# Kernel optimization log

Hardware: AMD Instinct MI355X
Metric: run time of the kernel (lower is better)

Reference implementation:

```python
import jax, jax.numpy as jnp
import numpy as np
import math

D_MODEL = 1024
D_STATE = 128
D_CONV = 4
EXPAND = 2
HEADDIM = 64
NGROUPS = 1
CHUNK = 256
D_INNER = EXPAND * D_MODEL
D_SSM = D_INNER
NHEADS = D_SSM // HEADDIM
CONV_DIM = D_SSM + 2 * NGROUPS * D_STATE
D_IN_PROJ = 2 * D_INNER + 2 * NGROUPS * D_STATE + NHEADS
BATCH = 2
SEQLEN = 4096
EPS = 1e-5


def segsum(x):
    # x: (..., T) -> (..., T, T); segsum[i, j] = sum_{j < k <= i} x[k], -inf above diagonal
    T = x.shape[-1]
    xc = jnp.cumsum(x, axis=-1)
    d = xc[..., :, None] - xc[..., None, :]
    mask = jnp.tril(jnp.ones((T, T), dtype=bool))
    return jnp.where(mask, d, -jnp.inf)


def setup_inputs() -> dict:
    key = jax.random.key(0)
    ks = jax.random.split(key, 8)
    u = jax.random.normal(ks[0], (BATCH, SEQLEN, D_MODEL), jnp.float32)
    W_in = jax.random.normal(ks[1], (D_IN_PROJ, D_MODEL), jnp.float32) / np.sqrt(D_MODEL)
    conv_w = jax.random.uniform(ks[2], (CONV_DIM, D_CONV), jnp.float32, -1.0, 1.0) / np.sqrt(D_CONV)
    conv_b = jnp.zeros((CONV_DIM,), jnp.float32)
    # dt_bias init as in the torch module: inverse-softplus of dt ~ LogUniform(1e-3, 1e-1)
    dt = jnp.exp(jax.random.uniform(ks[3], (NHEADS,), jnp.float32) * (math.log(0.1) - math.log(0.001)) + math.log(0.001))
    dt = jnp.maximum(dt, 1e-4)
    dt_bias = dt + jnp.log(-jnp.expm1(-dt))
    A_log = jnp.log(jax.random.uniform(ks[4], (NHEADS,), jnp.float32, 1.0, 16.0))
    D = jnp.ones((NHEADS,), jnp.float32)
    norm_w = jnp.ones((D_SSM,), jnp.float32)
    W_out = jax.random.normal(ks[5], (D_MODEL, D_INNER), jnp.float32) / np.sqrt(D_INNER)
    return {"u": u, "W_in": W_in, "conv_w": conv_w, "conv_b": conv_b,
            "dt_bias": dt_bias, "A_log": A_log, "D": D, "norm_w": norm_w, "W_out": W_out}


def reference(u, W_in, conv_w, conv_b, dt_bias, A_log, D, norm_w, W_out):
    b, L, _ = u.shape
    zxbcdt = u @ W_in.T  # (b, L, d_in_proj); d_mlp == 0 for this config
    z, xBC, dt = jnp.split(zxbcdt, [D_SSM, D_SSM + CONV_DIM], axis=-1)

    # depthwise causal conv1d + SiLU (kernel width D_CONV, left padding)
    xpad = jnp.pad(xBC, ((0, 0), (D_CONV - 1, 0), (0, 0)))
    acc = conv_b
    for k in range(D_CONV):
        acc = acc + xpad[:, k:k + L, :] * conv_w[:, k]
    xBC = jax.nn.silu(acc)

    x, Bm, Cm = jnp.split(xBC, [D_SSM, D_SSM + NGROUPS * D_STATE], axis=-1)
    hpg = NHEADS // NGROUPS  # heads per B/C group
    Bh = jnp.repeat(Bm.reshape(b, L, NGROUPS, D_STATE), hpg, axis=2)  # (b, L, h, n)
    Ch = jnp.repeat(Cm.reshape(b, L, NGROUPS, D_STATE), hpg, axis=2)
    x = x.reshape(b, L, NHEADS, HEADDIM)

    dt = jax.nn.softplus(dt + dt_bias)  # (b, L, h)
    A = -jnp.exp(A_log)  # (h,)

    # ---- SSD chunked selective scan ----
    nc = L // CHUNK
    xc = x.reshape(b, nc, CHUNK, NHEADS, HEADDIM)
    Bc = Bh.reshape(b, nc, CHUNK, NHEADS, D_STATE)
    Cc = Ch.reshape(b, nc, CHUNK, NHEADS, D_STATE)
    dt_bclh = dt.reshape(b, nc, CHUNK, NHEADS)
    dA = jnp.transpose(dt_bclh, (0, 3, 1, 2)) * A[None, :, None, None]  # (b, h, c, l)
    A_cs = jnp.cumsum(dA, axis=-1)  # (b, h, c, l)

    # intra-chunk (diagonal block) outputs
    Ldiag = jnp.exp(segsum(dA))  # (b, h, c, l, s)
    x_dt = xc * dt_bclh[..., None]  # fold dt into x
    Y_diag = jnp.einsum('bclhn,bcshn,bhcls,bcshp->bclhp', Cc, Bc, Ldiag, x_dt)

    # per-chunk final states
    decay_states = jnp.exp(A_cs[..., -1:] - A_cs)  # (b, h, c, l)
    states = jnp.einsum('bclhn,bhcl,bclhp->bchpn', Bc, decay_states, x_dt)

    # inter-chunk recurrence via segsum over chunk-level decays
    chunk_sum = jnp.pad(A_cs[..., -1], ((0, 0), (0, 0), (1, 0)))  # (b, h, c+1)
    decay_chunk = jnp.exp(segsum(chunk_sum))  # (b, h, c+1, c+1)
    states = jnp.concatenate([jnp.zeros_like(states[:, :1]), states], axis=1)
    new_states = jnp.einsum('bhzc,bchpn->bzhpn', decay_chunk, states)
    prev_states = new_states[:, :-1]  # state entering each chunk

    # state -> output contribution
    Y_off = jnp.einsum('bclhn,bchpn,bhcl->bclhp', Cc, prev_states, jnp.exp(A_cs))

    y = (Y_diag + Y_off).reshape(b, L, NHEADS, HEADDIM) + x * D[None, None, :, None]
    y = y.reshape(b, L, D_SSM)

    # gated RMSNorm (norm_before_gate=False, ngroups=1 -> full-dim norm)
    y = y * jax.nn.silu(z)
    y = y * jax.lax.rsqrt(jnp.mean(jnp.square(y), axis=-1, keepdims=True) + EPS) * norm_w
    return y @ W_out.T
```

## Files before the change

### kernel.cpp

```cpp
#include <hip/hip_runtime.h>
#include <hip/hip_bf16.h>

#define ZX_LD   4384
#define XC_LD   2304
#define NH      32
#define HD      64
#define DS      128
#define CHK     256
#define NC      16
#define LTOT    4096
#define ROWS    8192
#define DSSM    2048
#define YPAD    80

typedef __bf16 bf16_t;
typedef bf16_t bf16x8 __attribute__((ext_vector_type(8)));
typedef float  f32x4  __attribute__((ext_vector_type(4)));
typedef unsigned short u16x8 __attribute__((ext_vector_type(8)));
typedef unsigned short u16x4 __attribute__((ext_vector_type(4)));

__device__ inline float bf2f(unsigned short u) {
  unsigned int x = ((unsigned int)u) << 16;
  float f; __builtin_memcpy(&f, &x, 4); return f;
}

#define GLOAD_LDS16(gp, lp) \
  __builtin_amdgcn_global_load_lds((const __attribute__((address_space(1))) void*)(gp), \
                                   (__attribute__((address_space(3))) void*)(lp), 16, 0, 0)

__global__ __launch_bounds__(256) void cast_f32_bf16(
    const float* __restrict__ in, bf16_t* __restrict__ out,
    long nvalid, long total)
{
  const long e0 = ((long)blockIdx.x * 256 + threadIdx.x) * 8;
  if (e0 >= total) return;
  bf16x8 o;
  if (e0 + 8 <= nvalid) {
    const float4 a = *(const float4*)(in + e0);
    const float4 b = *(const float4*)(in + e0 + 4);
    o[0]=(bf16_t)a.x; o[1]=(bf16_t)a.y; o[2]=(bf16_t)a.z; o[3]=(bf16_t)a.w;
    o[4]=(bf16_t)b.x; o[5]=(bf16_t)b.y; o[6]=(bf16_t)b.z; o[7]=(bf16_t)b.w;
  } else {
#pragma unroll
    for (int j = 0; j < 8; ++j) o[j] = (bf16_t)0.f;
  }
  *(bf16x8*)(out + e0) = o;
}

__global__ __launch_bounds__(256) void gemm_bt_mfma(
    const bf16_t* __restrict__ A, const bf16_t* __restrict__ B,
    float* __restrict__ C, int M, int N, int K,
    int lda, int ldb, int ldc)
{
  __shared__ __align__(16) bf16_t As[128 * 32];
  __shared__ __align__(16) bf16_t Bs[128 * 32];
  const int tid  = threadIdx.x;
  const int lane = tid & 63;
  const int wave = tid >> 6;
  const int bm = blockIdx.y * 128;
  const int bn = blockIdx.x * 128;
  const int wr = (wave >> 1) * 64;
  const int wc = (wave & 1) * 64;

  const int c0   = wave * 2;
  const int lrow = lane >> 2;
  const int lcol = (lane & 3) * 8;
  const bf16_t* Ag0 = A + (size_t)(bm + c0 * 16 + lrow) * lda + lcol;
  const bf16_t* Ag1 = A + (size_t)(bm + c0 * 16 + 16 + lrow) * lda + lcol;
  const bf16_t* Bg0 = B + (size_t)(bn + c0 * 16 + lrow) * ldb + lcol;
  const bf16_t* Bg1 = B + (size_t)(bn + c0 * 16 + 16 + lrow) * ldb + lcol;
  bf16_t* Al0 = As + c0 * 512;
  bf16_t* Al1 = As + c0 * 512 + 512;
  bf16_t* Bl0 = Bs + c0 * 512;
  bf16_t* Bl1 = Bs + c0 * 512 + 512;

  f32x4 acc[4][4];
#pragma unroll
  for (int i = 0; i < 4; ++i)
#pragma unroll
    for (int j = 0; j < 4; ++j) acc[i][j] = (f32x4){0.f, 0.f, 0.f, 0.f};

  const int nk = K >> 5;
  for (int kt = 0; kt < nk; ++kt) {
    const int k0 = kt * 32;
    __syncthreads();
    GLOAD_LDS16(Ag0 + k0, Al0);
    GLOAD_LDS16(Ag1 + k0, Al1);
    GLOAD_LDS16(Bg0 + k0, Bl0);
    GLOAD_LDS16(Bg1 + k0, Bl1);
    __syncthreads();

    const bf16_t* Ab = As + (wr + (lane & 15)) * 32 + (lane >> 4) * 8;
    const bf16_t* Bb = Bs + (wc + (lane & 15)) * 32 + (lane >> 4) * 8;
    bf16x8 af[4], bfv[4];
#pragma unroll
    for (int mi = 0; mi < 4; ++mi) af[mi]  = *(const bf16x8*)(Ab + mi * 512);
#pragma unroll
    for (int ni = 0; ni < 4; ++ni) bfv[ni] = *(const bf16x8*)(Bb + ni * 512);
#pragma unroll
    for (int mi = 0; mi < 4; ++mi)
#pragma unroll
      for (int ni = 0; ni < 4; ++ni)
        acc[mi][ni] = __builtin_amdgcn_mfma_f32_16x16x32_bf16(af[mi], bfv[ni], acc[mi][ni], 0, 0, 0);
  }

  const int crow0 = bm + wr + (lane >> 4) * 4;
  const int ccol0 = bn + wc + (lane & 15);
#pragma unroll
  for (int ni = 0; ni < 4; ++ni) {
    const int ccol = ccol0 + ni * 16;
    if (ccol < N) {
#pragma unroll
      for (int mi = 0; mi < 4; ++mi) {
#pragma unroll
        for (int j = 0; j < 4; ++j) {
          C[(size_t)(crow0 + mi * 16 + j) * ldc + ccol] = acc[mi][ni][j];
        }
      }
    }
  }
}

__global__ __launch_bounds__(256) void conv_silu_kernel(
    const float* __restrict__ zx, const float* __restrict__ cw,
    const float* __restrict__ cb, bf16_t* __restrict__ xconv)
{
  const int ch  = blockIdx.x * 256 + threadIdx.x;
  const int row = blockIdx.y;
  const int l   = row & (LTOT - 1);
  float acc = cb[ch];
#pragma unroll
  for (int k = 0; k < 4; ++k) {
    const int ls = l - 3 + k;
    if (ls >= 0) acc = fmaf(zx[(size_t)(row - 3 + k) * ZX_LD + 2048 + ch], cw[ch*4 + k], acc);
  }
  const float r = acc / (1.f + __expf(-acc));
  xconv[(size_t)row * XC_LD + ch] = (bf16_t)r;
}

__global__ __launch_bounds__(256) void dt_kernel(
    const float* __restrict__ zx, const float* __restrict__ dtb,
    float* __restrict__ dtv)
{
  const int idx = blockIdx.x * 256 + threadIdx.x;
  const int row = idx >> 5;
  const int hh  = idx & 31;
  const float x = zx[(size_t)row * ZX_LD + 4352 + hh] + dtb[hh];
  dtv[idx] = (x > 20.f) ? x : log1pf(__expf(x));
}

__global__ __launch_bounds__(256) void chunk_states_kernel(
    const float* __restrict__ dtv, const float* __restrict__ A_log,
    const bf16_t* __restrict__ xconv,
    float* __restrict__ acs, float* __restrict__ totals,
    float* __restrict__ states)
{
  const int bid = blockIdx.x;
  const int h = bid & 31;
  const int c = (bid >> 5) & 15;
  const int b = bid >> 9;
  const int rowbase = b * LTOT + c * CHK;
  const int l = threadIdx.x;

  __shared__ float sWdt[256];
  __shared__ float wsum[4];
  __shared__ float xw[64][68];
  __shared__ float Bsh[64][132];

  const float dt = dtv[(size_t)(rowbase + l) * NH + h];
  const float Ah = -__expf(A_log[h]);
  float v = dt * Ah;
#pragma unroll
  for (int off = 1; off < 64; off <<= 1) {
    float up = __shfl_up(v, off, 64);
    if ((l & 63) >= off) v += up;
  }
  if ((l & 63) == 63) wsum[l >> 6] = v;
  __syncthreads();
  const float w0 = wsum[0], w1 = wsum[1], w2 = wsum[2], w3 = wsum[3];
  const int wid = l >> 6;
  float base = 0.f;
  if (wid > 0) base += w0;
  if (wid > 1) base += w1;
  if (wid > 2) base += w2;
  const float acsl  = v + base;
  const float total = w0 + w1 + w2 + w3;
  acs[bid * 256 + l] = acsl;
  if (l == 0) totals[(b * 32 + h) * 16 + c] = total;
  sWdt[l] = __expf(total - acsl) * dt;

  const int tx = l & 15;
  const int ty = l >> 4;
  const int r  = l >> 2;
  float acc[4][8];
#pragma unroll
  for (int i = 0; i < 4; ++i)
#pragma unroll
    for (int j = 0; j < 8; ++j) acc[i][j] = 0.f;

  for (int ls = 0; ls < 4; ++ls) {
    const int l0 = ls * 64;
    __syncthreads();
    {
      const float wgt = sWdt[l0 + r];
      const bf16_t* xrow = xconv + (size_t)(rowbase + l0 + r) * XC_LD + h * HD + (l & 3) * 16;
      float* xd = &xw[r][(l & 3) * 16];
      const u16x8* xp = (const u16x8*)xrow;
#pragma unroll
      for (int q = 0; q < 2; ++q) {
        u16x8 t = xp[q];
#pragma unroll
        for (int j = 0; j < 8; ++j) xd[q*8 + j] = bf2f(t[j]) * wgt;
      }
      const bf16_t* br = xconv + (size_t)(rowbase + l0 + r) * XC_LD + 2048 + (l & 3) * 32;
      float* bd = &Bsh[r][(l & 3) * 32];
      const u16x8* bp = (const u16x8*)br;
#pragma unroll
      for (int q = 0; q < 4; ++q) {
        u16x8 t = bp[q];
#pragma unroll
        for (int j = 0; j < 8; ++j) bd[q*8 + j] = bf2f(t[j]);
      }
    }
    __syncthreads();
#pragma unroll 8
    for (int s = 0; s < 64; ++s) {
      float4 pa = *(const float4*)&xw[s][ty*4];
      float4 b0 = *(const float4*)&Bsh[s][tx*4];
      float4 b1 = *(const float4*)&Bsh[s][64 + tx*4];
      float am[4] = {pa.x, pa.y, pa.z, pa.w};
      float bb[8] = {b0.x,b0.y,b0.z,b0.w,b1.x,b1.y,b1.z,b1.w};
#pragma unroll
      for (int i = 0; i < 4; ++i)
#pragma unroll
        for (int j = 0; j < 8; ++j) acc[i][j] = fmaf(am[i], bb[j], acc[i][j]);
    }
  }
  const size_t sbase = (size_t)bid * (HD * DS);
#pragma unroll
  for (int i = 0; i < 4; ++i) {
    const int p = ty * 4 + i;
#pragma unroll
    for (int j = 0; j < 8; ++j) {
      const int n = (j < 4) ? (tx*4 + j) : (64 + tx*4 + (j - 4));
      states[sbase + p * DS + n] = acc[i][j];
    }
  }
}

__global__ __launch_bounds__(256) void chunk_prefix_kernel(
    const float* __restrict__ st, const float* __restrict__ totals,
    bf16_t* __restrict__ prevbf)
{
  const int bh = blockIdx.x;
  const int b = bh >> 5;
  const int h = bh & 31;
  const int tid = threadIdx.x;
  float P[32];
#pragma unroll
  for (int e = 0; e < 32; ++e) P[e] = 0.f;
  for (int c = 0; c < NC; ++c) {
    const size_t base = (size_t)((b * 16 + c) * 32 + h) * (HD * DS);
    const float g = __expf(totals[bh * 16 + c]);
#pragma unroll
    for (int e = 0; e < 32; ++e) {
      const size_t idx = base + e * 256 + tid;
      prevbf[idx] = (bf16_t)P[e];
      P[e] = fmaf(P[e], g, st[idx]);
    }
  }
}

__global__ __launch_bounds__(256) void y_kernel_mfma(
    const bf16_t* __restrict__ xconv, const float* __restrict__ dtv,
    const float* __restrict__ acs,   const bf16_t* __restrict__ prevbf,
    const float* __restrict__ Dv,    float* __restrict__ ypre, int ypld)
{
  const int bid = blockIdx.x;
  const int lt = bid & 3;
  const int h  = (bid >> 2) & 31;
  const int c  = (bid >> 7) & 15;
  const int b  = bid >> 11;
  const int bch = (b * 16 + c) * 32 + h;
  const int rowbase = b * LTOT + c * CHK;
  const int tid  = threadIdx.x;
  const int lane = tid & 63;
  const int wv   = tid >> 6;
  const int ln15 = lane & 15;
  const int lg   = lane >> 4;

  __shared__ float sAcs[256];
  __shared__ float sDt[256];
  __shared__ __align__(16) bf16_t Cl[64 * 128];
  __shared__ __align__(16) bf16_t Bl[64 * 128];
  __shared__ __align__(16) bf16_t Sl[64 * YPAD];
  __shared__ __align__(16) bf16_t xT[64 * YPAD];
  unsigned short* xTu = (unsigned short*)xT;

  sAcs[tid] = acs[bch * 256 + tid];
  sDt[tid]  = dtv[(size_t)(rowbase + tid) * NH + h];

#pragma unroll
  for (int i = 0; i < 4; ++i) {
    const int chunk = wv * 4 + i;
    const int r  = chunk * 4 + lg;
    const int cs = ln15 ^ (r & 7);
    const bf16_t* src = xconv + (size_t)(rowbase + lt*64 + r) * XC_LD + 2176 + cs * 8;
    GLOAD_LDS16(src, Cl + chunk * 512);
  }
  __syncthreads();

  bf16x8 cf[4][4];
#pragma unroll
  for (int mi = 0; mi < 4; ++mi) {
    const int row = mi * 16 + ln15;
#pragma unroll
    for (int ks = 0; ks < 4; ++ks) {
      const int chunk = (ks * 4 + lg) ^ (row & 7);
      cf[mi][ks] = *(const bf16x8*)(Cl + row * 128 + chunk * 8);
    }
  }

  f32x4 acc[4];
#pragma unroll
  for (int mi = 0; mi < 4; ++mi) acc[mi] = (f32x4){0.f, 0.f, 0.f, 0.f};
  {
    const bf16_t* pb = prevbf + ((size_t)bch * 64 + 16 * wv + ln15) * 128 + lg * 8;
#pragma unroll
    for (int ks = 0; ks < 4; ++ks) {
      bf16x8 pf = *(const bf16x8*)(pb + ks * 32);
#pragma unroll
      for (int mi = 0; mi < 4; ++mi)
        acc[mi] = __builtin_amdgcn_mfma_f32_16x16x32_bf16(cf[mi][ks], pf, acc[mi], 0, 0, 0);
    }
  }
#pragma unroll
  for (int mi = 0; mi < 4; ++mi) {
#pragma unroll
    for (int j = 0; j < 4; ++j)
      acc[mi][j] *= __expf(sAcs[lt*64 + mi*16 + lg*4 + j]);
  }

  for (int st = 0; st <= lt; ++st) {
    __syncthreads();
#pragma unroll
    for (int i = 0; i < 4; ++i) {
      const int chunk = wv * 4 + i;
      const int r  = chunk * 4 + lg;
      const int cs = ln15 ^ (r & 7);
      const bf16_t* src = xconv + (size_t)(rowbase + st*64 + r) * XC_LD + 2048 + cs * 8;
      GLOAD_LDS16(src, Bl + chunk * 512);
    }
    {
      const int s  = tid >> 2;
      const int p0 = (tid & 3) * 16;
      const bf16_t* xr = xconv + (size_t)(rowbase + st*64 + s) * XC_LD + h * HD + p0;
      u16x8 v0 = *(const u16x8*)xr;
      u16x8 v1 = *(const u16x8*)(xr + 8);
#pragma unroll
      for (int j = 0; j < 8; ++j) xTu[(p0 + j) * YPAD + s] = v0[j];
#pragma unroll
      for (int j = 0; j < 8; ++j) xTu[(p0 + 8 + j) * YPAD + s] = v1[j];
    }
    __syncthreads();

    f32x4 sa[4];
#pragma unroll
    for (int mi = 0; mi < 4; ++mi) sa[mi] = (f32x4){0.f, 0.f, 0.f, 0.f};
    {
      const int row = 16 * wv + ln15;
#pragma unroll
      for (int ks = 0; ks < 4; ++ks) {
        const int chunk = (ks * 4 + lg) ^ (row & 7);
        bf16x8 bfr = *(const bf16x8*)(Bl + row * 128 + chunk * 8);
#pragma unroll
        for (int mi = 0; mi < 4; ++mi)
          sa[mi] = __builtin_amdgcn_mfma_f32_16x16x32_bf16(cf[mi][ks], bfr, sa[mi], 0, 0, 0);
      }
    }
    {
      const int sg = st * 64 + 16 * wv + ln15;
      const float as  = sAcs[sg];
      const float dts = sDt[sg];
#pragma unroll
      for (int mi = 0; mi < 4; ++mi) {
#pragma unroll
        for (int j = 0; j < 4; ++j) {
          const int lloc = mi * 16 + lg * 4 + j;
          const int ll = lt * 64 + lloc;
          float wvv = 0.f;
          if (ll >= sg) wvv = sa[mi][j] * __expf(sAcs[ll] - as) * dts;
          Sl[lloc * YPAD + 16 * wv + ln15] = (bf16_t)wvv;
        }
      }
    }
    __syncthreads();

#pragma unroll
    for (int ks2 = 0; ks2 < 2; ++ks2) {
      bf16x8 xf = *(const bf16x8*)(xT + (16 * wv + ln15) * YPAD + ks2 * 32 + lg * 8);
#pragma unroll
      for (int mi = 0; mi < 4; ++mi) {
        bf16x8 sf = *(const bf16x8*)(Sl + (mi * 16 + ln15) * YPAD + ks2 * 32 + lg * 8);
        acc[mi] = __builtin_amdgcn_mfma_f32_16x16x32_bf16(sf, xf, acc[mi], 0, 0, 0);
      }
    }
  }

  const float Dh = Dv[h];
  const int p = 16 * wv + ln15;
#pragma unroll
  for (int mi = 0; mi < 4; ++mi) {
#pragma unroll
    for (int j = 0; j < 4; ++j) {
      const int lloc = mi * 16 + lg * 4 + j;
      const int row  = rowbase + lt * 64 + lloc;
      const float xv = (float)xT[p * YPAD + lloc];
      ypre[(size_t)row * ypld + h * HD + p] = acc[mi][j] + xv * Dh;
    }
  }
}

__global__ __launch_bounds__(256) void rmsnorm_gate_kernel(
    const float* __restrict__ zx, const float* __restrict__ normw,
    bf16_t* __restrict__ ypre_bf)
{
  const int row = blockIdx.x;
  const int tid = threadIdx.x;
  float vals[8];
  float ss = 0.f;
#pragma unroll
  for (int e = 0; e < 8; ++e) {
    const int col = e * 256 + tid;
    const float y = zx[(size_t)row * ZX_LD + 2048 + col];
    const float z = zx[(size_t)row * ZX_LD + col];
    const float sz = z / (1.f + __expf(-z));
    const float v = y * sz;
    vals[e] = v;
    ss += v * v;
  }
#pragma unroll
  for (int off = 32; off >= 1; off >>= 1) ss += __shfl_xor(ss, off, 64);
  __shared__ float red[4];
  if ((tid & 63) == 0) red[tid >> 6] = ss;
  __syncthreads();
  const float tot = red[0] + red[1] + red[2] + red[3];
  const float scale = rsqrtf(tot / (float)DSSM + 1e-5f);
#pragma unroll
  for (int e = 0; e < 8; ++e) {
    const int col = e * 256 + tid;
    ypre_bf[(size_t)row * DSSM + col] = (bf16_t)(vals[e] * scale * normw[col]);
  }
}

extern "C" void kernel_launch(void* const* d_in, const int* in_sizes, int n_in,
                              void* d_out, int out_size, void* d_ws, size_t ws_size,
                              hipStream_t stream)
{
  const float* u       = (const float*)d_in[0];
  const float* W_in    = (const float*)d_in[1];
  const float* conv_w  = (const float*)d_in[2];
  const float* conv_b  = (const float*)d_in[3];
  const float* dt_bias = (const float*)d_in[4];
  const float* A_log   = (const float*)d_in[5];
  const float* Dv      = (const float*)d_in[6];
  const float* norm_w  = (const float*)d_in[7];
  const float* W_out   = (const float*)d_in[8];
  float* out = (float*)d_out;

  const size_t OFF_XC  = (size_t)ROWS * ZX_LD * 4;
  const size_t OFF_DT  = OFF_XC  + (size_t)ROWS * XC_LD * 2;
  const size_t OFF_ACS = OFF_DT  + (size_t)ROWS * NH * 4;
  const size_t OFF_TOT = OFF_ACS + (size_t)1024 * 256 * 4;
  const size_t OFF_ST  = OFF_TOT + 4096;
  const size_t OFF_AR  = OFF_ST  + (size_t)1024 * HD * DS * 4;
  const size_t need    = OFF_AR  + (size_t)ROWS * XC_LD * 2;
  if (ws_size < need) return;

  char* w = (char*)d_ws;
  float*  zx      = (float*)w;
  bf16_t* xconv   = (bf16_t*)(w + OFF_XC);
  float*  dtv     = (float*)(w + OFF_DT);
  float*  acsb    = (float*)(w + OFF_ACS);
  float*  totals  = (float*)(w + OFF_TOT);
  float*  states  = (float*)(w + OFF_ST);
  bf16_t* arena   = (bf16_t*)(w + OFF_AR);
  bf16_t* u_bf    = arena;
  bf16_t* Wpad    = arena + (size_t)ROWS * 1024;
  bf16_t* prevbf  = arena;
  bf16_t* ypre_bf = arena;
  bf16_t* Wout_bf = arena + (size_t)ROWS * DSSM;
  float*  ypre    = zx + 2048;

  {
    const long n_u = (long)ROWS * 1024;
    cast_f32_bf16<<<dim3((n_u/8 + 255)/256), 256, 0, stream>>>(u, u_bf, n_u, n_u);
    const long n_wv = (long)4384 * 1024, n_wt = (long)4480 * 1024;
    cast_f32_bf16<<<dim3((n_wt/8 + 255)/256), 256, 0, stream>>>(W_in, Wpad, n_wv, n_wt);
    const long n_wo = (long)1024 * DSSM;
    cast_f32_bf16<<<dim3((n_wo/8 + 255)/256), 256, 0, stream>>>(W_out, Wout_bf, n_wo, n_wo);
  }
  gemm_bt_mfma<<<dim3(35, 64), 256, 0, stream>>>(u_bf, Wpad, zx, ROWS, 4384, 1024,
                                                 1024, 1024, ZX_LD);
  conv_silu_kernel<<<dim3(9, ROWS), 256, 0, stream>>>(zx, conv_w, conv_b, xconv);
  dt_kernel<<<dim3((ROWS * NH) / 256), 256, 0, stream>>>(zx, dt_bias, dtv);
  chunk_states_kernel<<<dim3(1024), 256, 0, stream>>>(dtv, A_log, xconv, acsb, totals, states);
  chunk_prefix_kernel<<<dim3(64), 256, 0, stream>>>(states, totals, prevbf);
  y_kernel_mfma<<<dim3(4096), 256, 0, stream>>>(xconv, dtv, acsb, prevbf, Dv, ypre, ZX_LD);
  rmsnorm_gate_kernel<<<dim3(ROWS), 256, 0, stream>>>(zx, norm_w, ypre_bf);
  gemm_bt_mfma<<<dim3(8, 64), 256, 0, stream>>>(ypre_bf, Wout_bf, out, ROWS, 1024, 2048,
                                                2048, 2048, 1024);
}
```

Before: 587.4 us.

## Use MFMA for chunk states, parallelize prefix scan, remap GEMM tiles per XCD

Result: faster. 525.2 us (-10.6%).

```diff
diff --git a/kernel.cpp b/kernel.cpp
--- a/kernel.cpp
+++ b/kernel.cpp
@@ -57,8 +57,17 @@
   const int tid  = threadIdx.x;
   const int lane = tid & 63;
   const int wave = tid >> 6;
-  const int bm = blockIdx.y * 128;
-  const int bn = blockIdx.x * 128;
+
+  const int nwg  = gridDim.x * gridDim.y;
+  int wgid = blockIdx.y * gridDim.x + blockIdx.x;
+  {
+    const int xcd = wgid & 7, local = wgid >> 3;
+    const int q = nwg >> 3, r = nwg & 7;
+    wgid = (xcd < r ? xcd * (q + 1) : r * (q + 1) + (xcd - r) * q) + local;
+  }
+  const int bm = (wgid / gridDim.x) * 128;
+  const int bn = (wgid % gridDim.x) * 128;
+
   const int wr = (wave >> 1) * 64;
   const int wc = (wave & 1) * 64;
 
@@ -160,90 +169,111 @@
   const int c = (bid >> 5) & 15;
   const int b = bid >> 9;
   const int rowbase = b * LTOT + c * CHK;
-  const int l = threadIdx.x;
+  const int tid = threadIdx.x;
+  const int lane = tid & 63;
+  const int wv   = tid >> 6;
+  const int ln15 = lane & 15;
+  const int lg   = lane >> 4;
 
   __shared__ float sWdt[256];
   __shared__ float wsum[4];
-  __shared__ float xw[64][68];
-  __shared__ float Bsh[64][132];
-
-  const float dt = dtv[(size_t)(rowbase + l) * NH + h];
+  __shared__ __align__(16) bf16_t xT[64 * 64];
+  __shared__ __align__(16) bf16_t Bt[128 * 64];
+  unsigned short* Btu = (unsigned short*)Bt;
+
+  const float dt = dtv[(size_t)(rowbase + tid) * NH + h];
   const float Ah = -__expf(A_log[h]);
   float v = dt * Ah;
 #pragma unroll
   for (int off = 1; off < 64; off <<= 1) {
     float up = __shfl_up(v, off, 64);
-    if ((l & 63) >= off) v += up;
-  }
-  if ((l & 63) == 63) wsum[l >> 6] = v;
+    if ((tid & 63) >= off) v += up;
+  }
+  if ((tid & 63) == 63) wsum[tid >> 6] = v;
   __syncthreads();
   const float w0 = wsum[0], w1 = wsum[1], w2 = wsum[2], w3 = wsum[3];
-  const int wid = l >> 6;
   float base = 0.f;
-  if (wid > 0) base += w0;
-  if (wid > 1) base += w1;
-  if (wid > 2) base += w2;
+  if (wv > 0) base += w0;
+  if (wv > 1) base += w1;
+  if (wv > 2) base += w2;
   const float acsl  = v + base;
   const float total = w0 + w1 + w2 + w3;
-  acs[bid * 256 + l] = acsl;
-  if (l == 0) totals[(b * 32 + h) * 16 + c] = total;
-  sWdt[l] = __expf(total - acsl) * dt;
-
-  const int tx = l & 15;
-  const int ty = l >> 4;
-  const int r  = l >> 2;
-  float acc[4][8];
+  acs[bid * 256 + tid] = acsl;
+  if (tid == 0) totals[(b * 32 + h) * 16 + c] = total;
+  sWdt[tid] = __expf(total - acsl) * dt;
+
+  f32x4 acc[4][2];
 #pragma unroll
   for (int i = 0; i < 4; ++i)
 #pragma unroll
-    for (int j = 0; j < 8; ++j) acc[i][j] = 0.f;
+    for (int j = 0; j < 2; ++j) acc[i][j] = (f32x4){0.f, 0.f, 0.f, 0.f};
+
+  const int s  = tid >> 2;
+  const int p0 = (tid & 3) * 16;
+  const int n0 = (tid & 3) * 32;
 
   for (int ls = 0; ls < 4; ++ls) {
     const int l0 = ls * 64;
     __syncthreads();
     {
-      const float wgt = sWdt[l0 + r];
-      const bf16_t* xrow = xconv + (size_t)(rowbase + l0 + r) * XC_LD + h * HD + (l & 3) * 16;
-      float* xd = &xw[r][(l & 3) * 16];
-      const u16x8* xp = (const u16x8*)xrow;
-#pragma unroll
-      for (int q = 0; q < 2; ++q) {
-        u16x8 t = xp[q];
-#pragma unroll
-        for (int j = 0; j < 8; ++j) xd[q*8 + j] = bf2f(t[j]) * wgt;
-      }
-      const bf16_t* br = xconv + (size_t)(rowbase + l0 + r) * XC_LD + 2048 + (l & 3) * 32;
-      float* bd = &Bsh[r][(l & 3) * 32];
-      const u16x8* bp = (const u16x8*)br;
+      const float wgt = sWdt[l0 + s];
+      const bf16_t* xr = xconv + (size_t)(rowbase + l0 + s) * XC_LD + h * HD + p0;
+      u16x8 v0 = *(const u16x8*)xr;
+      u16x8 v1 = *(const u16x8*)(xr + 8);
+#pragma unroll
+      for (int j = 0; j < 8; ++j) {
+        const int p = p0 + j;
+        xT[p * 64 + ((((s >> 3) ^ (p & 7)) << 3) | (s & 7))] = (bf16_t)(bf2f(v0[j]) * wgt);
+      }
+#pragma unroll
+      for (int j = 0; j < 8; ++j) {
+        const int p = p0 + 8 + j;
+        xT[p * 64 + ((((s >> 3) ^ (p & 7)) << 3) | (s & 7))] = (bf16_t)(bf2f(v1[j]) * wgt);
+      }
+      const bf16_t* br = xconv + (size_t)(rowbase + l0 + s) * XC_LD + 2048 + n0;
 #pragma unroll
       for (int q = 0; q < 4; ++q) {
-        u16x8 t = bp[q];
-#pragma unroll
-        for (int j = 0; j < 8; ++j) bd[q*8 + j] = bf2f(t[j]);
-      }
-    }
-    __syncthreads();
-#pragma unroll 8
-    for (int s = 0; s < 64; ++s) {
-      float4 pa = *(const float4*)&xw[s][ty*4];
-      float4 b0 = *(const float4*)&Bsh[s][tx*4];
-      float4 b1 = *(const float4*)&Bsh[s][64 + tx*4];
-      float am[4] = {pa.x, pa.y, pa.z, pa.w};
-      float bb[8] = {b0.x,b0.y,b0.z,b0.w,b1.x,b1.y,b1.z,b1.w};
-#pragma unroll
-      for (int i = 0; i < 4; ++i)
-#pragma unroll
-        for (int j = 0; j < 8; ++j) acc[i][j] = fmaf(am[i], bb[j], acc[i][j]);
-    }
-  }
+        u16x8 t = *(const u16x8*)(br + q * 8);
+#pragma unroll
+        for (int j = 0; j < 8; ++j) {
+          const int n = n0 + q * 8 + j;
+          Btu[n * 64 + ((((s >> 3) ^ (n & 7)) << 3) | (s & 7))] = t[j];
+        }
+      }
+    }
+    __syncthreads();
+#pragma unroll
+    for (int ks = 0; ks < 2; ++ks) {
+      bf16x8 af[4];
+#pragma unroll
+      for (int mi = 0; mi < 4; ++mi) {
+        const int row = mi * 16 + ln15;
+        const int chunk = (ks * 4 + lg) ^ (row & 7);
+        af[mi] = *(const bf16x8*)(xT + row * 64 + chunk * 8);
+      }
+#pragma unroll
+      for (int ni = 0; ni < 2; ++ni) {
+        const int nrow = wv * 32 + ni * 16 + ln15;
+        const int chunk = (ks * 4 + lg) ^ (nrow & 7);
+        bf16x8 bfr = *(const bf16x8*)(Bt + nrow * 64 + chunk * 8);
+#pragma unroll
+        for (int mi = 0; mi < 4; ++mi)
+          acc[mi][ni] = __builtin_amdgcn_mfma_f32_16x16x32_bf16(af[mi], bfr, acc[mi][ni], 0, 0, 0);
+      }
+    }
+  }
+
   const size_t sbase = (size_t)bid * (HD * DS);
 #pragma unroll
-  for (int i = 0; i < 4; ++i) {
-    const int p = ty * 4 + i;
-#pragma unroll
-    for (int j = 0; j < 8; ++j) {
-      const int n = (j < 4) ? (tx*4 + j) : (64 + tx*4 + (j - 4));
-      states[sbase + p * DS + n] = acc[i][j];
+  for (int mi = 0; mi < 4; ++mi) {
+#pragma unroll
+    for (int ni = 0; ni < 2; ++ni) {
+      const int n = wv * 32 + ni * 16 + ln15;
+#pragma unroll
+      for (int j = 0; j < 4; ++j) {
+        const int p = mi * 16 + lg * 4 + j;
+        states[sbase + p * DS + n] = acc[mi][ni][j];
+      }
     }
   }
 }
@@ -255,19 +285,14 @@
   const int bh = blockIdx.x;
   const int b = bh >> 5;
   const int h = bh & 31;
+  const int e = blockIdx.y;
   const int tid = threadIdx.x;
-  float P[32];
-#pragma unroll
-  for (int e = 0; e < 32; ++e) P[e] = 0.f;
+  float P = 0.f;
   for (int c = 0; c < NC; ++c) {
-    const size_t base = (size_t)((b * 16 + c) * 32 + h) * (HD * DS);
+    const size_t idx = (size_t)((b * 16 + c) * 32 + h) * (HD * DS) + e * 256 + tid;
     const float g = __expf(totals[bh * 16 + c]);
-#pragma unroll
-    for (int e = 0; e < 32; ++e) {
-      const size_t idx = base + e * 256 + tid;
-      prevbf[idx] = (bf16_t)P[e];
-      P[e] = fmaf(P[e], g, st[idx]);
-    }
+    prevbf[idx] = (bf16_t)P;
+    P = fmaf(P, g, st[idx]);
   }
 }
 
@@ -505,7 +530,7 @@
   conv_silu_kernel<<<dim3(9, ROWS), 256, 0, stream>>>(zx, conv_w, conv_b, xconv);
   dt_kernel<<<dim3((ROWS * NH) / 256), 256, 0, stream>>>(zx, dt_bias, dtv);
   chunk_states_kernel<<<dim3(1024), 256, 0, stream>>>(dtv, A_log, xconv, acsb, totals, states);
-  chunk_prefix_kernel<<<dim3(64), 256, 0, stream>>>(states, totals, prevbf);
+  chunk_prefix_kernel<<<dim3(64, 32), 256, 0, stream>>>(states, totals, prevbf);
   y_kernel_mfma<<<dim3(4096), 256, 0, stream>>>(xconv, dtv, acsb, prevbf, Dv, ypre, ZX_LD);
   rmsnorm_gate_kernel<<<dim3(ROWS), 256, 0, stream>>>(zx, norm_w, ypre_bf);
   gemm_bt_mfma<<<dim3(8, 64), 256, 0, stream>>>(ypre_bf, Wout_bf, out, ROWS, 1024, 2048,
```
